# Performance work log

Measured on AMD Instinct MI355X. Metric: run time of the kernel, lower is better.

Reference implementation:

```python
import jax, jax.numpy as jnp
import numpy as np

EPS = 1e-5
K = 5  # sklearn NearestNeighbors(n_neighbors=5); includes the query point itself


def setup_inputs() -> dict:
    key = jax.random.key(0)
    points = jax.random.uniform(key, (16384, 3), dtype=jnp.float32)
    return {"points": points}


def _compute_lrfs(points):
    # Brute-force KNN (indices only; sklearn returns the self-point as nearest).
    sq = jnp.sum(points * points, axis=1)                      # [N]
    d2 = sq[:, None] + sq[None, :] - 2.0 * points @ points.T   # [N,N]
    _, nbh_idx = jax.lax.top_k(-jax.lax.stop_gradient(d2), K)  # [N,K] (indices only -> no grad path)

    diffs = points[nbh_idx] - points[:, None, :]               # [N,K,3]  (nbh = points[idx] - point)
    centered = diffs - diffs.mean(axis=1, keepdims=True)
    cov = jnp.einsum('nkd,nke->nde', centered, centered) / K   # torch.cov(nbh.T, correction=0)
    eigvals, eigvecs = jnp.linalg.eigh(cov)                    # ascending eigvals, [N,3],[N,3,3]
    order = jnp.argsort(eigvals, axis=-1)[:, ::-1]             # descending

    # NOTE faithful quirks of the original:
    #  - eigvecs.T[:, axis] == eigvecs[axis, :] -> ROW of eigvecs is used as the axis
    #  - _calc_axis receives nbh (already point-relative) and does (pt - point) again,
    #    so the vote uses (neighbor - 2*point) dotted with the axis.
    def axis_row(idx):
        v = jnp.take_along_axis(eigvecs, idx[:, None, None], axis=1)[:, 0, :]  # [N,3]
        vote_vec = diffs - points[:, None, :]                                  # [N,K,3]
        count = jnp.sum(jnp.einsum('nkd,nd->nk', vote_vec, v) >= -EPS, axis=1)
        sign = jnp.where(2 * count >= K, 1.0, -1.0).astype(points.dtype)       # count >= K/2 keeps
        return v * sign[:, None]

    x_axis = axis_row(order[:, 0])
    z_axis = axis_row(order[:, 2])
    y_axis = jnp.cross(z_axis, x_axis)
    return jnp.stack([x_axis, y_axis, z_axis], axis=1)  # [N,3,3]


def reference(points):
    # forward(points, return_lrfs=True) -> (shot=0, lrfs); return the lrfs (the only real output).
    return _compute_lrfs(points)
```

## Files before the change

kernel.cpp:

```cpp
#include <hip/hip_runtime.h>

#define SLARTG_NEW 1

namespace {

constexpr int KNN_K = 5;
constexpr int GRID = 16;
constexpr int CELLS = GRID * GRID * GRID;
constexpr int LPG = 8;

constexpr int PPB = 16;
constexpr int STR = 16;
constexpr int TPB = PPB * STR;
constexpr int TILE = 2048;

#define EPSF    5.9604644775390625e-8f
#define EPS2F   3.552713678800501e-15f
#define SAFMINF 1.1754943508222875e-38f
#define SAFMAXF 8.507059173023462e+37f
#define RTMINF  1.0842021724855044e-19f
#define RTMAXF  9.223372036854776e+18f

__device__ __forceinline__ float sqnorm3(float x, float y, float z) {
#pragma clang fp contract(off)
  float a = x * x;
  float b = y * y;
  float c = z * z;
  return (a + b) + c;
}

__device__ __forceinline__ float dist2(float xi, float yi, float zi, float sqi,
                                       float xj, float yj, float zj, float sqj) {
#pragma clang fp contract(off)
  float dot = (xi * xj + yi * yj) + zi * zj;
  float a = sqi + sqj;
  return a - 2.0f * dot;
}

__device__ __forceinline__ int cell1d(float v) {
  int c = (int)(v * (float)GRID);
  if (c < 0) c = 0;
  if (c > GRID - 1) c = GRID - 1;
  return c;
}

__device__ __forceinline__ float slapy2f(float x, float y) {
#pragma clang fp contract(off)
  float xa = fabsf(x), ya = fabsf(y);
  float w = fmaxf(xa, ya);
  float z = fminf(xa, ya);
  if (z == 0.f) return w;
  float q = z / w;
  float q2 = q * q;
  float s = 1.0f + q2;
  return w * sqrtf(s);
}

__device__ __forceinline__ void slartgf(float f, float g, float* cs, float* sn, float* r) {
#pragma clang fp contract(off)
#if SLARTG_NEW
  float f1 = fabsf(f), g1 = fabsf(g);
  if (g == 0.f) { *cs = 1.f; *sn = 0.f; *r = f; }
  else if (f == 0.f) { *cs = 0.f; *sn = copysignf(1.f, g); *r = g1; }
  else if (f1 > RTMINF && f1 < RTMAXF && g1 > RTMINF && g1 < RTMAXF) {
    float ff = f * f;
    float gg = g * g;
    float d = sqrtf(ff + gg);
    *cs = f1 / d;
    float rr = copysignf(d, f);
    *sn = g / rr;
    *r = rr;
  } else {
    float u = fminf(SAFMAXF, fmaxf(fmaxf(SAFMINF, f1), g1));
    float fs = f / u, gs = g / u;
    float ff = fs * fs;
    float gg = gs * gs;
    float d = sqrtf(ff + gg);
    *cs = fabsf(fs) / d;
    float rr = copysignf(d, f);
    *sn = gs / rr;
    *r = rr * u;
  }
#else
  if (g == 0.f) { *cs = 1.f; *sn = 0.f; *r = f; }
  else if (f == 0.f) { *cs = 0.f; *sn = 1.f; *r = g; }
  else {
    float f2 = f * f;
    float g2 = g * g;
    float rr = sqrtf(f2 + g2);
    float c = f / rr, s = g / rr;
    if (fabsf(f) > fabsf(g) && c < 0.f) { c = -c; s = -s; rr = -rr; }
    *cs = c; *sn = s; *r = rr;
  }
#endif
}

__device__ __forceinline__ void slaev2f(float a, float b, float c,
                                        float* rt1, float* rt2, float* cs1, float* sn1) {
#pragma clang fp contract(off)
  float sm = a + c;
  float df = a - c;
  float adf = fabsf(df);
  float tb = b + b;
  float ab = fabsf(tb);
  float acmx, acmn;
  if (fabsf(a) > fabsf(c)) { acmx = a; acmn = c; } else { acmx = c; acmn = a; }
  float rt;
  if (adf > ab) { float q = ab / adf; rt = adf * sqrtf(1.0f + q * q); }
  else if (adf < ab) { float q = adf / ab; rt = ab * sqrtf(1.0f + q * q); }
  else rt = ab * sqrtf(2.0f);
  int sgn1;
  if (sm < 0.f) { *rt1 = 0.5f * (sm - rt); sgn1 = -1; *rt2 = (acmx / *rt1) * acmn - (b / *rt1) * b; }
  else if (sm > 0.f) { *rt1 = 0.5f * (sm + rt); sgn1 = 1; *rt2 = (acmx / *rt1) * acmn - (b / *rt1) * b; }
  else { *rt1 = 0.5f * rt; *rt2 = -0.5f * rt; sgn1 = 1; }
  float cs; int sgn2;
  if (df >= 0.f) { cs = df + rt; sgn2 = 1; } else { cs = df - rt; sgn2 = -1; }
  float acs = fabsf(cs);
  float c1, s1;
  if (acs > ab) {
    float ct = -tb / cs;
    s1 = 1.0f / sqrtf(1.0f + ct * ct);
    c1 = ct * s1;
  } else {
    if (ab == 0.f) { c1 = 1.f; s1 = 0.f; }
    else {
      float tn = -cs / tb;
      c1 = 1.0f / sqrtf(1.0f + tn * tn);
      s1 = tn * c1;
    }
  }
  if (sgn1 == sgn2) { float tn = c1; c1 = -s1; s1 = tn; }
  *cs1 = c1; *sn1 = s1;
}

__device__ __forceinline__ void slascl_g(float cfrom, float cto, int n, float* a) {
#pragma clang fp contract(off)
  float cfromc = cfrom, ctoc = cto;
  bool done = false;
  int guard = 0;
  while (!done && guard++ < 50) {
    float mul;
    float cfrom1 = cfromc * SAFMINF;
    if (cfrom1 == cfromc) {
      mul = ctoc / cfromc; done = true;
    } else {
      float cto1 = ctoc / SAFMAXF;
      if (cto1 == ctoc) { mul = ctoc; done = true; cfromc = 1.f; }
      else if (fabsf(cfrom1) > fabsf(ctoc) && ctoc != 0.f) { mul = SAFMINF; done = false; cfromc = cfrom1; }
      else if (fabsf(cto1) > fabsf(cfromc)) { mul = SAFMAXF; done = false; ctoc = cto1; }
      else { mul = ctoc / cfromc; done = true; }
    }
    for (int i = 0; i < n; ++i) a[i] = a[i] * mul;
  }
}

__device__ void steqr3f(float* d, float* e, float Z[3][3]) {
#pragma clang fp contract(off)
  const int n = 3;
  const float eps = EPSF, eps2 = EPS2F, safmin = SAFMINF;
  const float ssfmax = sqrtf(SAFMAXF) / 3.0f;
  const float ssfmin = sqrtf(SAFMINF) / EPS2F;
  int jtot = 0; const int nmaxit = n * 30;
  int l1 = 1;

  for (int guard = 0; guard < 200; ++guard) {
    if (l1 > n) break;
    if (l1 > 1) e[l1 - 2] = 0.f;
    int m = n;
    if (l1 <= n - 1) {
      for (int q = l1; q <= n - 1; ++q) {
        float tst = fabsf(e[q - 1]);
        if (tst == 0.f) { m = q; break; }
        if (tst <= (sqrtf(fabsf(d[q - 1])) * sqrtf(fabsf(d[q]))) * eps) { e[q - 1] = 0.f; m = q; break; }
      }
    }
    int l = l1, lsv = l, lend = m, lendsv = lend;
    l1 = m + 1;
    if (lend == l) continue;
    float anorm = 0.f;
    for (int q = l; q <= lend; ++q) anorm = fmaxf(anorm, fabsf(d[q - 1]));
    for (int q = l; q <= lend - 1; ++q) anorm = fmaxf(anorm, fabsf(e[q - 1]));
    int iscale = 0;
    if (anorm == 0.f) continue;
    if (anorm > ssfmax) {
      iscale = 1;
      slascl_g(anorm, ssfmax, lend - l + 1, d + l - 1);
      slascl_g(anorm, ssfmax, lend - l, e + l - 1);
    } else if (anorm < ssfmin) {
      iscale = 2;
      slascl_g(anorm, ssfmin, lend - l + 1, d + l - 1);
      slascl_g(anorm, ssfmin, lend - l, e + l - 1);
    }
    if (fabsf(d[lend - 1]) < fabsf(d[l - 1])) { lend = lsv; l = lendsv; }

    if (lend > l) {
      for (int g2 = 0; g2 < 400; ++g2) {
        int mm = lend;
        if (l != lend) {
          bool fnd = false;
          for (int q = l; q <= lend - 1; ++q) {
            float tst = e[q - 1] * e[q - 1];
            if (tst <= (eps2 * fabsf(d[q - 1])) * fabsf(d[q]) + safmin) { mm = q; fnd = true; break; }
          }
          if (!fnd) mm = lend;
        }
        if (mm < lend) e[mm - 1] = 0.f;
        float p = d[l - 1];
        if (mm == l) {
          d[l - 1] = p; ++l;
          if (l <= lend) continue; else break;
        }
        if (mm == l + 1) {
          float rt1, rt2, c, s;
          slaev2f(d[l - 1], e[l - 1], d[l], &rt1, &rt2, &c, &s);
          for (int r2 = 0; r2 < 3; ++r2) {
            float zt = Z[r2][l];
            float zl = Z[r2][l - 1];
            Z[r2][l] = c * zt - s * zl;
            Z[r2][l - 1] = s * zt + c * zl;
          }
          d[l - 1] = rt1; d[l] = rt2; e[l - 1] = 0.f;
          l += 2;
          if (l <= lend) continue; else break;
        }
        if (jtot == nmaxit) break;
        ++jtot;
        float g = (d[l] - p) / (2.0f * e[l - 1]);
        float r = slapy2f(g, 1.0f);
        g = d[mm - 1] - p + e[l - 1] / (g + copysignf(r, g));
        float ss = 1.0f, cc = 1.0f;
        p = 0.f;
        float cw[2], sw[2];
        for (int q = mm - 1; q >= l; --q) {
          float f = ss * e[q - 1];
          float b = cc * e[q - 1];
          float rr;
          slartgf(g, f, &cc, &ss, &rr);
          if (q != mm - 1) e[q] = rr;
          g = d[q] - p;
          rr = (d[q - 1] - g) * ss + 2.0f * cc * b;
          p = ss * rr;
          d[q] = g + p;
          g = cc * rr - b;
          cw[q - l] = cc; sw[q - l] = -ss;
        }
        for (int q = mm - 1; q >= l; --q) {
          float cj = cw[q - l], sj = sw[q - l];
          for (int r2 = 0; r2 < 3; ++r2) {
            float zt = Z[r2][q];
            float zl = Z[r2][q - 1];
            Z[r2][q] = cj * zt - sj * zl;
            Z[r2][q - 1] = sj * zt + cj * zl;
          }
        }
        d[l - 1] = d[l - 1] - p;
        e[l - 1] = g;
      }
    } else {
      for (int g2 = 0; g2 < 400; ++g2) {
        int mm = lend;
        if (l != lend) {
          bool fnd = false;
          for (int q = l; q >= lend + 1; --q) {
            float tst = e[q - 2] * e[q - 2];
            if (tst <= (eps2 * fabsf(d[q - 1])) * fabsf(d[q - 2]) + safmin) { mm = q; fnd = true; break; }
          }
          if (!fnd) mm = lend;
        }
        if (mm > lend) e[mm - 2] = 0.f;
        float p = d[l - 1];
        if (mm == l) {
          d[l - 1] = p; --l;
          if (l >= lend) continue; else break;
        }
        if (mm == l - 1) {
          float rt1, rt2, c, s;
          slaev2f(d[l - 2], e[l - 2], d[l - 1], &rt1, &rt2, &c, &s);
          for (int r2 = 0; r2 < 3; ++r2) {
            float zt = Z[r2][l - 1];
            float zl = Z[r2][l - 2];
            Z[r2][l - 1] = c * zt - s * zl;
            Z[r2][l - 2] = s * zt + c * zl;
          }
          d[l - 2] = rt1; d[l - 1] = rt2; e[l - 2] = 0.f;
          l -= 2;
          if (l >= lend) continue; else break;
        }
        if (jtot == nmaxit) break;
        ++jtot;
        float g = (d[l - 2] - p) / (2.0f * e[l - 2]);
        float r = slapy2f(g, 1.0f);
        g = d[mm - 1] - p + e[l - 2] / (g + copysignf(r, g));
        float ss = 1.0f, cc = 1.0f;
        p = 0.f;
        float cw[2], sw[2];
        for (int q = mm; q <= l - 1; ++q) {
          float f = ss * e[q - 1];
          float b = cc * e[q - 1];
          float rr;
          slartgf(g, f, &cc, &ss, &rr);
          if (q != mm) e[q - 2] = rr;
          g = d[q - 1] - p;
          rr = (d[q] - g) * ss + 2.0f * cc * b;
          p = ss * rr;
          d[q - 1] = g + p;
          g = cc * rr - b;
          cw[q - mm] = cc; sw[q - mm] = ss;
        }
        for (int q = mm; q <= l - 1; ++q) {
          float cj = cw[q - mm], sj = sw[q - mm];
          for (int r2 = 0; r2 < 3; ++r2) {
            float zt = Z[r2][q];
            float zl = Z[r2][q - 1];
            Z[r2][q] = cj * zt - sj * zl;
            Z[r2][q - 1] = sj * zt + cj * zl;
          }
        }
        d[l - 1] = d[l - 1] - p;
        e[l - 2] = g;
      }
    }
    if (iscale == 1) {
      slascl_g(ssfmax, anorm, lendsv - lsv + 1, d + lsv - 1);
      slascl_g(ssfmax, anorm, lendsv - lsv, e + lsv - 1);
    } else if (iscale == 2) {
      slascl_g(ssfmin, anorm, lendsv - lsv + 1, d + lsv - 1);
      slascl_g(ssfmin, anorm, lendsv - lsv, e + lsv - 1);
    }
    if (jtot >= nmaxit) break;
  }
  for (int ii = 2; ii <= n; ++ii) {
    int i0 = ii - 1, k0 = i0;
    float p = d[i0 - 1];
    for (int j = ii; j <= n; ++j)
      if (d[j - 1] < p) { k0 = j; p = d[j - 1]; }
    if (k0 != i0) {
      d[k0 - 1] = d[i0 - 1]; d[i0 - 1] = p;
      for (int r2 = 0; r2 < 3; ++r2) {
        float t = Z[r2][i0 - 1]; Z[r2][i0 - 1] = Z[r2][k0 - 1]; Z[r2][k0 - 1] = t;
      }
    }
  }
}

__device__ __forceinline__ float vote5(const float dif[KNN_K][3],
                                       float px, float py, float pz, const float v[3]) {
#pragma clang fp contract(off)
  int cnt = 0;
  for (int k = 0; k < KNN_K; ++k) {
    float w0 = dif[k][0] - px;
    float w1 = dif[k][1] - py;
    float w2 = dif[k][2] - pz;
    float dt = (w0 * v[0] + w1 * v[1]) + w2 * v[2];
    cnt += (dt >= -1e-5f) ? 1 : 0;
  }
  return (2 * cnt >= KNN_K) ? 1.0f : -1.0f;
}

__device__ __forceinline__ void lrf_one(const float* __restrict__ P, float* __restrict__ out,
                                        int i, int n0, int n1, int n2, int n3, int n4) {
#pragma clang fp contract(off)
  int nb[KNN_K] = {n0, n1, n2, n3, n4};
  float px = P[i * 3 + 0], py = P[i * 3 + 1], pz = P[i * 3 + 2];
  float dif[KNN_K][3];
#pragma unroll
  for (int k = 0; k < KNN_K; ++k) {
    int j = nb[k];
    dif[k][0] = P[j * 3 + 0] - px;
    dif[k][1] = P[j * 3 + 1] - py;
    dif[k][2] = P[j * 3 + 2] - pz;
  }
  float mean[3];
  for (int c = 0; c < 3; ++c) {
    float sm = dif[0][c];
    for (int k = 1; k < KNN_K; ++k) sm = sm + dif[k][c];
    mean[c] = sm / 5.0f;
  }
  float cen[KNN_K][3];
  for (int k = 0; k < KNN_K; ++k)
    for (int c = 0; c < 3; ++c) cen[k][c] = dif[k][c] - mean[c];
  float cov[3][3];
  for (int a = 0; a < 3; ++a)
    for (int b = 0; b < 3; ++b) {
      float sm = cen[0][a] * cen[0][b];
      for (int k = 1; k < KNN_K; ++k) sm = sm + cen[k][a] * cen[k][b];
      cov[a][b] = sm / 5.0f;
    }

  float a00 = cov[0][0], a10 = cov[1][0], a20 = cov[2][0];
  float a11 = cov[1][1], a21 = cov[2][1], a22 = cov[2][2];
  float dd[3], ee[2];
  float taui = 0.f, v2 = 0.f;
  float xnorm = fabsf(a20);
  if (xnorm == 0.f) {
    taui = 0.f;
    ee[0] = a10;
    dd[0] = a00; dd[1] = a11; dd[2] = a22; ee[1] = a21;
  } else {
    float beta = -copysignf(slapy2f(a10, xnorm), a10);
    taui = (beta - a10) / beta;
    v2 = a20 * (1.0f / (a10 - beta));
    ee[0] = beta;
    float w1 = taui * a11 + taui * (a21 * v2);
    float w2 = taui * a21 + (taui * v2) * a22;
    float dot = w1 + w2 * v2;
    float al = -((0.5f * taui) * dot);
    w1 = w1 + al;
    w2 = w2 + al * v2;
    dd[1] = (a11 - w1) - w1;
    ee[1] = (a21 - (v2 * w1)) - w2;
    dd[2] = (a22 - (v2 * w2)) - (w2 * v2);
    dd[0] = a00;
  }

  float Zm[3][3] = {{1.f, 0.f, 0.f}, {0.f, 1.f, 0.f}, {0.f, 0.f, 1.f}};
  steqr3f(dd, ee, Zm);

  if (taui != 0.f) {
    for (int j = 0; j < 3; ++j) {
      float w = Zm[1][j] + v2 * Zm[2][j];
      float t = -(taui * w);
      Zm[1][j] = Zm[1][j] + t;
      Zm[2][j] = Zm[2][j] + v2 * t;
    }
  }

  float vx[3] = {Zm[2][0], Zm[2][1], Zm[2][2]};
  float vz[3] = {Zm[0][0], Zm[0][1], Zm[0][2]};
  float sx = vote5(dif, px, py, pz, vx);
  float sz = vote5(dif, px, py, pz, vz);
  float X[3] = {vx[0] * sx, vx[1] * sx, vx[2] * sx};
  float Zx[3] = {vz[0] * sz, vz[1] * sz, vz[2] * sz};
  float Y[3] = {Zx[1] * X[2] - Zx[2] * X[1],
                Zx[2] * X[0] - Zx[0] * X[2],
                Zx[0] * X[1] - Zx[1] * X[0]};
  out[i * 9 + 0] = X[0]; out[i * 9 + 1] = X[1]; out[i * 9 + 2] = X[2];
  out[i * 9 + 3] = Y[0]; out[i * 9 + 4] = Y[1]; out[i * 9 + 5] = Y[2];
  out[i * 9 + 6] = Zx[0]; out[i * 9 + 7] = Zx[1]; out[i * 9 + 8] = Zx[2];
}

#define LT(d1, i1, d2, i2) ((d1) < (d2) || ((d1) == (d2) && (i1) < (i2)))

struct Top5 {
  float d0, d1, d2, d3, d4;
  int j0, j1, j2, j3, j4;

  __device__ __forceinline__ void init() {
    d0 = d1 = d2 = d3 = d4 = 1e30f;
    j0 = j1 = j2 = j3 = j4 = 0x7fffffff;
  }

  __device__ __forceinline__ void insert(float dv, int j) {
    if (!LT(dv, j, d4, j4)) return;
    bool l3 = LT(dv, j, d3, j3);
    bool l2 = LT(dv, j, d2, j2);
    bool l1 = LT(dv, j, d1, j1);
    bool l0 = LT(dv, j, d0, j0);
    d4 = l3 ? d3 : dv;              j4 = l3 ? j3 : j;
    d3 = l3 ? (l2 ? d2 : dv) : d3;  j3 = l3 ? (l2 ? j2 : j) : j3;
    d2 = l2 ? (l1 ? d1 : dv) : d2;  j2 = l2 ? (l1 ? j1 : j) : j2;
    d1 = l1 ? (l0 ? d0 : dv) : d1;  j1 = l1 ? (l0 ? j0 : j) : j1;
    d0 = l0 ? dv : d0;              j0 = l0 ? j : j0;
  }

  __device__ __forceinline__ void merge_xor(int off) {
    float pd0 = __shfl_xor(d0, off), pd1 = __shfl_xor(d1, off),
          pd2 = __shfl_xor(d2, off), pd3 = __shfl_xor(d3, off),
          pd4 = __shfl_xor(d4, off);
    int pj0 = __shfl_xor(j0, off), pj1 = __shfl_xor(j1, off),
        pj2 = __shfl_xor(j2, off), pj3 = __shfl_xor(j3, off),
        pj4 = __shfl_xor(j4, off);
    insert(pd0, pj0); insert(pd1, pj1); insert(pd2, pj2);
    insert(pd3, pj3); insert(pd4, pj4);
  }
};


__global__ __launch_bounds__(256) void hist_kernel(
    const float* __restrict__ P, int* __restrict__ counts, int n) {
  int i = blockIdx.x * 256 + threadIdx.x;
  if (i >= n) return;
  int cx = cell1d(P[i * 3 + 0]);
  int cy = cell1d(P[i * 3 + 1]);
  int cz = cell1d(P[i * 3 + 2]);
  atomicAdd(&counts[(cz * GRID + cy) * GRID + cx], 1);
}

__global__ __launch_bounds__(256) void scan_kernel(
    int* __restrict__ counts ,
    int* __restrict__ cursor) {
  __shared__ int psum[256];
  const int tid = threadIdx.x;
  const int CHUNK = CELLS / 256;
  int local[CHUNK];
  int s = 0;
  for (int k = 0; k < CHUNK; ++k) {
    local[k] = s;
    s += counts[tid * CHUNK + k];
  }
  psum[tid] = s;
  __syncthreads();
  for (int off = 1; off < 256; off <<= 1) {
    int v = (tid >= off) ? psum[tid - off] : 0;
    __syncthreads();
    psum[tid] += v;
    __syncthreads();
  }
  int base = (tid > 0) ? psum[tid - 1] : 0;
  for (int k = 0; k < CHUNK; ++k) {
    int o = base + local[k];
    counts[tid * CHUNK + k] = o;
    cursor[tid * CHUNK + k] = o;
  }
  if (tid == 255) counts[CELLS] = psum[255];
}

__global__ __launch_bounds__(256) void scatter_kernel(
    const float* __restrict__ P, int* __restrict__ cursor,
    float4* __restrict__ sorted, int n) {
  int i = blockIdx.x * 256 + threadIdx.x;
  if (i >= n) return;
  float x = P[i * 3 + 0], y = P[i * 3 + 1], z = P[i * 3 + 2];
  int c = (cell1d(z) * GRID + cell1d(y)) * GRID + cell1d(x);
  int pos = atomicAdd(&cursor[c], 1);
  sorted[pos] = make_float4(x, y, z, __int_as_float(i));
}

__global__ __launch_bounds__(256) void knn_kernel(
    const float4* __restrict__ sorted, const int* __restrict__ offsets,
    int* __restrict__ nbh, int n) {
  const int tid = threadIdx.x;
  const int r = tid & (LPG - 1);
  const int t = blockIdx.x * (256 / LPG) + (tid / LPG);
  if (t >= n) return;

  float4 q = sorted[t];
  const float qs = sqnorm3(q.x, q.y, q.z);
  const int cx = cell1d(q.x), cy = cell1d(q.y), cz = cell1d(q.z);
  const float h = 1.0f / (float)GRID;

  Top5 tp;
  tp.init();

  {
    const int x0 = max(0, cx - 1), x1 = min(GRID - 1, cx + 1);
    const int xsp = x1 - x0 + 1;
    int ksv[9], kev[9];
#pragma unroll
    for (int s9 = 0; s9 < 9; ++s9) {
      int dz = s9 / 3 - 1, dy = s9 % 3 - 1;
      int zz = cz + dz, yy = cy + dy;
      bool ok = (zz >= 0) && (zz < GRID) && (yy >= 0) && (yy < GRID);
      int c0 = ok ? ((zz * GRID + yy) * GRID + x0) : 0;
      int ks = offsets[c0];
      int ke = offsets[c0 + xsp];
      ksv[s9] = ks;
      kev[s9] = ok ? ke : ks;
    }
#pragma unroll
    for (int s9 = 0; s9 < 9; ++s9) {
      for (int k = ksv[s9] + r; k < kev[s9]; k += LPG) {
        float4 p = sorted[k];
        float psq = sqnorm3(p.x, p.y, p.z);
        float dv = dist2(q.x, q.y, q.z, qs, p.x, p.y, p.z, psq);
        tp.insert(dv, __float_as_int(p.w));
      }
    }
  }

  float B = tp.d4;
  B = fminf(B, __shfl_xor(B, 1));
  B = fminf(B, __shfl_xor(B, 2));
  B = fminf(B, __shfl_xor(B, 4));

  for (int m = 2; m < GRID; ++m) {
    float lb = (float)(m - 1) * h;
    if (lb * lb > B * 1.00001f + 1e-6f) break;
    for (int dz = -m; dz <= m; ++dz) {
      int zz = cz + dz;
      if (zz < 0 || zz >= GRID) continue;
      bool zface = (dz == -m || dz == m);
      for (int dy = -m; dy <= m; ++dy) {
        int yy = cy + dy;
        if (yy < 0 || yy >= GRID) continue;
        bool yface = (dy == -m || dy == m);
        int rowbase = (zz * GRID + yy) * GRID;
        if (zface || yface) {
          int x0 = max(0, cx - m), x1 = min(GRID - 1, cx + m);
          int ks = offsets[rowbase + x0], ke = offsets[rowbase + x1 + 1];
          for (int k = ks + r; k < ke; k += LPG) {
            float4 p = sorted[k];
            float psq = sqnorm3(p.x, p.y, p.z);
            float dv = dist2(q.x, q.y, q.z, qs, p.x, p.y, p.z, psq);
            tp.insert(dv, __float_as_int(p.w));
          }
        } else {
          int xa = cx - m, xb = cx + m;
          if (xa >= 0) {
            int ks = offsets[rowbase + xa], ke = offsets[rowbase + xa + 1];
            for (int k = ks + r; k < ke; k += LPG) {
              float4 p = sorted[k];
              float psq = sqnorm3(p.x, p.y, p.z);
              float dv = dist2(q.x, q.y, q.z, qs, p.x, p.y, p.z, psq);
              tp.insert(dv, __float_as_int(p.w));
            }
          }
          if (xb < GRID) {
            int ks = offsets[rowbase + xb], ke = offsets[rowbase + xb + 1];
            for (int k = ks + r; k < ke; k += LPG) {
              float4 p = sorted[k];
              float psq = sqnorm3(p.x, p.y, p.z);
              float dv = dist2(q.x, q.y, q.z, qs, p.x, p.y, p.z, psq);
              tp.insert(dv, __float_as_int(p.w));
            }
          }
        }
      }
    }
    B = tp.d4;
    B = fminf(B, __shfl_xor(B, 1));
    B = fminf(B, __shfl_xor(B, 2));
    B = fminf(B, __shfl_xor(B, 4));
  }

  tp.merge_xor(1);
  tp.merge_xor(2);
  tp.merge_xor(4);

  if (r == 0) {
    nbh[t * 5 + 0] = tp.j0;
    nbh[t * 5 + 1] = tp.j1;
    nbh[t * 5 + 2] = tp.j2;
    nbh[t * 5 + 3] = tp.j3;
    nbh[t * 5 + 4] = tp.j4;
  }
}

__global__ __launch_bounds__(64) void solver_kernel(
    const float* __restrict__ P, const float4* __restrict__ sorted,
    const int* __restrict__ nbh, float* __restrict__ out, int n) {
  int t = blockIdx.x * 64 + threadIdx.x;
  if (t >= n) return;
  int io = __float_as_int(sorted[t].w);
  lrf_one(P, out, io,
          nbh[t * 5 + 0], nbh[t * 5 + 1], nbh[t * 5 + 2],
          nbh[t * 5 + 3], nbh[t * 5 + 4]);
}


__global__ __launch_bounds__(TPB) void knn_brute_kernel(
    const float* __restrict__ P, float* __restrict__ out, int n) {
  __shared__ float4 tile[TILE];

  const int tid = threadIdx.x;
  const int p = tid >> 4;
  const int s = tid & 15;
  const int i = blockIdx.x * PPB + p;
  const int iq = (i < n) ? i : (n - 1);

  const float qx = P[iq * 3 + 0];
  const float qy = P[iq * 3 + 1];
  const float qz = P[iq * 3 + 2];
  const float qs = sqnorm3(qx, qy, qz);

  Top5 t;
  t.init();

  for (int base = 0; base < n; base += TILE) {
    int cnt = min(TILE, n - base);
    __syncthreads();
    for (int j = tid; j < cnt; j += TPB) {
      float x = P[(base + j) * 3 + 0];
      float y = P[(base + j) * 3 + 1];
      float z = P[(base + j) * 3 + 2];
      tile[j] = make_float4(x, y, z, sqnorm3(x, y, z));
    }
    __syncthreads();
    for (int j = s; j < cnt; j += STR) {
      float4 q = tile[j];
      t.insert(dist2(qx, qy, qz, qs, q.x, q.y, q.z, q.w), base + j);
    }
  }

#pragma unroll
  for (int rnd = 0; rnd < 4; ++rnd) {
    t.merge_xor(1 << rnd);
  }

  if (s == 0 && i < n) {
    lrf_one(P, out, i, t.j0, t.j1, t.j2, t.j3, t.j4);
  }
}

}

extern "C" void kernel_launch(void* const* d_in, const int* in_sizes, int n_in,
                              void* d_out, int out_size, void* d_ws, size_t ws_size,
                              hipStream_t stream) {
  (void)n_in; (void)out_size;
  const float* P = (const float*)d_in[0];
  float* out = (float*)d_out;
  const int n = in_sizes[0] / 3;
  if (n <= 0) return;

  size_t off_sorted = 0;
  size_t off_counts = off_sorted + (size_t)n * sizeof(float4);
  size_t off_cursor = off_counts + ((size_t)(CELLS + 1) * sizeof(int) + 15) / 16 * 16;
  size_t off_nbh = off_cursor + (size_t)CELLS * sizeof(int);
  size_t need = off_nbh + (size_t)n * 5 * sizeof(int);

  if (ws_size >= need && n >= KNN_K) {
    char* base = (char*)d_ws;
    float4* sorted = (float4*)(base + off_sorted);
    int* counts = (int*)(base + off_counts);
    int* cursor = (int*)(base + off_cursor);
    int* nbh = (int*)(base + off_nbh);

    hipMemsetAsync(counts, 0, (size_t)CELLS * sizeof(int), stream);
    hist_kernel<<<(n + 255) / 256, 256, 0, stream>>>(P, counts, n);
    scan_kernel<<<1, 256, 0, stream>>>(counts, cursor);
    scatter_kernel<<<(n + 255) / 256, 256, 0, stream>>>(P, cursor, sorted, n);
    const int ppb = 256 / LPG;
    knn_kernel<<<(n + ppb - 1) / ppb, 256, 0, stream>>>(sorted, counts, nbh, n);
    solver_kernel<<<(n + 63) / 64, 64, 0, stream>>>(P, sorted, nbh, out, n);
  } else {
    const int blocks = (n + PPB - 1) / PPB;
    knn_brute_kernel<<<blocks, TPB, 0, stream>>>(P, out, n);
  }
}
```

Measured before the change: 107.7 us.

## Split KNN into ring-0/1 pass and queued full-wave ring-2+ refinement

```diff
diff --git a/kernel.cpp b/kernel.cpp
--- a/kernel.cpp
+++ b/kernel.cpp
@@ -526,9 +526,10 @@
   sorted[pos] = make_float4(x, y, z, __int_as_float(i));
 }
 
-__global__ __launch_bounds__(256) void knn_kernel(
+__global__ __launch_bounds__(256) void knn_ring01_kernel(
     const float4* __restrict__ sorted, const int* __restrict__ offsets,
-    int* __restrict__ nbh, int n) {
+    int* __restrict__ nbh, int* __restrict__ queue, int* __restrict__ qcount,
+    int n) {
   const int tid = threadIdx.x;
   const int r = tid & (LPG - 1);
   const int t = blockIdx.x * (256 / LPG) + (tid / LPG);
@@ -568,14 +569,54 @@
     }
   }
 
-  float B = tp.d4;
-  B = fminf(B, __shfl_xor(B, 1));
-  B = fminf(B, __shfl_xor(B, 2));
-  B = fminf(B, __shfl_xor(B, 4));
+  tp.merge_xor(1);
+  tp.merge_xor(2);
+  tp.merge_xor(4);
+
+  if (r == 0) {
+    nbh[t * 5 + 0] = tp.j0;
+    nbh[t * 5 + 1] = tp.j1;
+    nbh[t * 5 + 2] = tp.j2;
+    nbh[t * 5 + 3] = tp.j3;
+    nbh[t * 5 + 4] = tp.j4;
+    if (!(h * h > tp.d4 * 1.00001f + 1e-6f)) {
+      int qi = atomicAdd(qcount, 1);
+      queue[qi] = t;
+    }
+  }
+}
+
+__global__ __launch_bounds__(64) void knn_ring2_kernel(
+    const float4* __restrict__ sorted, const int* __restrict__ offsets,
+    const float* __restrict__ P, const int* __restrict__ queue,
+    const int* __restrict__ qcount, int* __restrict__ nbh, int n) {
+  const int wv = blockIdx.x;
+  if (wv >= *qcount) return;
+  const int t = queue[wv];
+  const int lane = threadIdx.x;
+
+  float4 q = sorted[t];
+  const float qs = sqnorm3(q.x, q.y, q.z);
+  const int cx = cell1d(q.x), cy = cell1d(q.y), cz = cell1d(q.z);
+  const float h = 1.0f / (float)GRID;
+
+  Top5 tp;
+  tp.init();
+  if (lane == 0) {
+#pragma unroll
+    for (int k = 0; k < 5; ++k) {
+      int j = nbh[t * 5 + k];
+      float xj = P[j * 3 + 0], yj = P[j * 3 + 1], zj = P[j * 3 + 2];
+      float sj = sqnorm3(xj, yj, zj);
+      float dv = dist2(q.x, q.y, q.z, qs, xj, yj, zj, sj);
+      tp.insert(dv, j);
+    }
+  }
+  float B4 = __shfl(tp.d4, 0);
 
   for (int m = 2; m < GRID; ++m) {
     float lb = (float)(m - 1) * h;
-    if (lb * lb > B * 1.00001f + 1e-6f) break;
+    if (lb * lb > B4 * 1.00001f + 1e-6f) break;
     for (int dz = -m; dz <= m; ++dz) {
       int zz = cz + dz;
       if (zz < 0 || zz >= GRID) continue;
@@ -588,7 +629,7 @@
         if (zface || yface) {
           int x0 = max(0, cx - m), x1 = min(GRID - 1, cx + m);
           int ks = offsets[rowbase + x0], ke = offsets[rowbase + x1 + 1];
-          for (int k = ks + r; k < ke; k += LPG) {
+          for (int k = ks + lane; k < ke; k += 64) {
             float4 p = sorted[k];
             float psq = sqnorm3(p.x, p.y, p.z);
             float dv = dist2(q.x, q.y, q.z, qs, p.x, p.y, p.z, psq);
@@ -598,7 +639,7 @@
           int xa = cx - m, xb = cx + m;
           if (xa >= 0) {
             int ks = offsets[rowbase + xa], ke = offsets[rowbase + xa + 1];
-            for (int k = ks + r; k < ke; k += LPG) {
+            for (int k = ks + lane; k < ke; k += 64) {
               float4 p = sorted[k];
               float psq = sqnorm3(p.x, p.y, p.z);
               float dv = dist2(q.x, q.y, q.z, qs, p.x, p.y, p.z, psq);
@@ -607,7 +648,7 @@
           }
           if (xb < GRID) {
             int ks = offsets[rowbase + xb], ke = offsets[rowbase + xb + 1];
-            for (int k = ks + r; k < ke; k += LPG) {
+            for (int k = ks + lane; k < ke; k += 64) {
               float4 p = sorted[k];
               float psq = sqnorm3(p.x, p.y, p.z);
               float dv = dist2(q.x, q.y, q.z, qs, p.x, p.y, p.z, psq);
@@ -617,17 +658,16 @@
         }
       }
     }
-    B = tp.d4;
-    B = fminf(B, __shfl_xor(B, 1));
-    B = fminf(B, __shfl_xor(B, 2));
-    B = fminf(B, __shfl_xor(B, 4));
-  }
-
-  tp.merge_xor(1);
-  tp.merge_xor(2);
-  tp.merge_xor(4);
-
-  if (r == 0) {
+    tp.merge_xor(1);
+    tp.merge_xor(2);
+    tp.merge_xor(4);
+    tp.merge_xor(8);
+    tp.merge_xor(16);
+    tp.merge_xor(32);
+    B4 = tp.d4;
+  }
+
+  if (lane == 0) {
     nbh[t * 5 + 0] = tp.j0;
     nbh[t * 5 + 1] = tp.j1;
     nbh[t * 5 + 2] = tp.j2;
@@ -707,7 +747,9 @@
   size_t off_counts = off_sorted + (size_t)n * sizeof(float4);
   size_t off_cursor = off_counts + ((size_t)(CELLS + 1) * sizeof(int) + 15) / 16 * 16;
   size_t off_nbh = off_cursor + (size_t)CELLS * sizeof(int);
-  size_t need = off_nbh + (size_t)n * 5 * sizeof(int);
+  size_t off_queue = off_nbh + (size_t)n * 5 * sizeof(int);
+  size_t off_qcount = off_queue + (size_t)n * sizeof(int);
+  size_t need = off_qcount + 16;
 
   if (ws_size >= need && n >= KNN_K) {
     char* base = (char*)d_ws;
@@ -715,13 +757,18 @@
     int* counts = (int*)(base + off_counts);
     int* cursor = (int*)(base + off_cursor);
     int* nbh = (int*)(base + off_nbh);
+    int* queue = (int*)(base + off_queue);
+    int* qcount = (int*)(base + off_qcount);
 
     hipMemsetAsync(counts, 0, (size_t)CELLS * sizeof(int), stream);
+    hipMemsetAsync(qcount, 0, sizeof(int), stream);
     hist_kernel<<<(n + 255) / 256, 256, 0, stream>>>(P, counts, n);
     scan_kernel<<<1, 256, 0, stream>>>(counts, cursor);
     scatter_kernel<<<(n + 255) / 256, 256, 0, stream>>>(P, cursor, sorted, n);
     const int ppb = 256 / LPG;
-    knn_kernel<<<(n + ppb - 1) / ppb, 256, 0, stream>>>(sorted, counts, nbh, n);
+    knn_ring01_kernel<<<(n + ppb - 1) / ppb, 256, 0, stream>>>(
+        sorted, counts, nbh, queue, qcount, n);
+    knn_ring2_kernel<<<n, 64, 0, stream>>>(sorted, counts, P, queue, qcount, nbh, n);
     solver_kernel<<<(n + 63) / 64, 64, 0, stream>>>(P, sorted, nbh, out, n);
   } else {
     const int blocks = (n + PPB - 1) / PPB;
```

New measurement: 123.3 us. 14.4% more time.
